# Kernel optimization log

Hardware: AMD Instinct MI355X
Metric: run time of the kernel (lower is better)

## Reference

```python
import math
import jax, jax.numpy as jnp
import numpy as np

EMBED_DIM = 2048
NUM_HEADS = 16
NUM_KV_HEADS = 8
DEPTH = 12
HEAD_DIM = EMBED_DIM // NUM_HEADS // 2  # 64
N_REP = NUM_HEADS // NUM_KV_HEADS       # 2
SCALING = HEAD_DIM ** (-0.5)
LAMBDA_INIT = 0.8 - 0.6 * math.exp(-0.3 * DEPTH)
EPS = 1e-5


def _rope_cos_sin(seq_len, head_dim, offset=0):
    pos = jnp.arange(offset, offset + seq_len, dtype=jnp.float32)
    theta = jnp.arange(0, head_dim, 2, dtype=jnp.float32) / head_dim
    inv_freq = 1.0 / (10000.0 ** theta + 1e-8)
    sinusoid = pos[:, None] * inv_freq[None, :]  # [seq, head_dim//2]
    return jnp.cos(sinusoid), jnp.sin(sinusoid)


def _apply_rotary_interleaved(x, cos, sin):
    # x: [b, s, h, d]; cos/sin: [s, d//2]; interleaved pairs (even, odd)
    x1 = x[..., 0::2]
    x2 = x[..., 1::2]
    c = cos[None, :, None, :]
    s = sin[None, :, None, :]
    o1 = x1 * c - x2 * s
    o2 = x1 * s + x2 * c
    return jnp.stack([o1, o2], axis=-1).reshape(x.shape)


def setup_inputs() -> dict:
    key = jax.random.key(0)
    ks = jax.random.split(key, 12)
    d = EMBED_DIM
    inp = {
        "q": jax.random.normal(ks[0], (1, 2048, d), dtype=jnp.float32),
        "k": jax.random.normal(ks[1], (1, 2048, d), dtype=jnp.float32),
        "v": jax.random.normal(ks[2], (1, 2048, d), dtype=jnp.float32),
        "Wq": jax.random.normal(ks[3], (d, d), dtype=jnp.float32) * (d ** -0.5),
        "Wk": jax.random.normal(ks[4], (d, d // N_REP), dtype=jnp.float32) * (d ** -0.5),
        "Wv": jax.random.normal(ks[5], (d, d // N_REP), dtype=jnp.float32) * (d ** -0.5),
        "Wout": jax.random.normal(ks[6], (d, d), dtype=jnp.float32) * (d ** -0.5),
        "lq1": jax.random.normal(ks[7], (HEAD_DIM,), dtype=jnp.float32) * 0.1,
        "lk1": jax.random.normal(ks[8], (HEAD_DIM,), dtype=jnp.float32) * 0.1,
        "lq2": jax.random.normal(ks[9], (HEAD_DIM,), dtype=jnp.float32) * 0.1,
        "lk2": jax.random.normal(ks[10], (HEAD_DIM,), dtype=jnp.float32) * 0.1,
        "subln_w": jnp.ones((2 * HEAD_DIM,), dtype=jnp.float32),
    }
    return inp


def reference(q, k, v, Wq, Wk, Wv, Wout, lq1, lk1, lq2, lk2, subln_w):
    bsz, tgt_len, _ = q.shape
    src_len = k.shape[1]
    hd = HEAD_DIM

    qp = (q @ Wq).reshape(bsz, tgt_len, 2 * NUM_HEADS, hd)
    kp = (k @ Wk).reshape(bsz, src_len, 2 * NUM_KV_HEADS, hd)
    vp = (v @ Wv).reshape(bsz, src_len, NUM_KV_HEADS, 2 * hd)

    q_cos, q_sin = _rope_cos_sin(tgt_len, hd)
    k_cos, k_sin = _rope_cos_sin(src_len, hd)
    qp = _apply_rotary_interleaved(qp, q_cos, q_sin)
    kp = _apply_rotary_interleaved(kp, k_cos, k_sin)

    qp = jnp.transpose(qp, (0, 2, 1, 3)) * SCALING          # [b, 2H, t, hd]
    kp = jnp.repeat(jnp.transpose(kp, (0, 2, 1, 3)), N_REP, axis=1)  # [b, 2H, s, hd]
    vp = jnp.repeat(jnp.transpose(vp, (0, 2, 1, 3)), N_REP, axis=1)  # [b, H, s, 2hd]

    attn_weights = jnp.einsum('bhtd,bhsd->bhts', qp, kp)
    attn_weights = jax.nn.softmax(attn_weights.astype(jnp.float32), axis=-1).astype(qp.dtype)

    lambda_1 = jnp.exp(jnp.sum(lq1 * lk1))
    lambda_2 = jnp.exp(jnp.sum(lq2 * lk2))
    lambda_full = lambda_1 - lambda_2 + LAMBDA_INIT

    attn_weights = attn_weights.reshape(bsz, NUM_HEADS, 2, tgt_len, src_len)
    attn_weights = attn_weights[:, :, 0] - lambda_full * attn_weights[:, :, 1]

    attn = jnp.einsum('bhts,bhsd->bhtd', attn_weights, vp)  # [b, H, t, 2hd]

    # RMSNorm over last dim with affine weight
    rms = jax.lax.rsqrt(jnp.mean(jnp.square(attn), axis=-1, keepdims=True) + EPS)
    attn = attn * rms * subln_w
    attn = attn * (1.0 - LAMBDA_INIT)

    attn = jnp.transpose(attn, (0, 2, 1, 3)).reshape(bsz, tgt_len, NUM_HEADS * 2 * hd)
    return attn @ Wout
```

## Files before the change

kernel.cpp:

```cpp
#include <hip/hip_runtime.h>

typedef unsigned short u16;
typedef unsigned int u32;
typedef float f32x4 __attribute__((ext_vector_type(4)));
typedef float f32x2 __attribute__((ext_vector_type(2)));
typedef unsigned int u32x2 __attribute__((ext_vector_type(2)));
typedef __bf16 bf16x8 __attribute__((ext_vector_type(8)));
typedef __bf16 bf16x4 __attribute__((ext_vector_type(4)));

#define LAMBDA_INIT_F 0.7836057665316245f
#define ONE_MINUS_LI  0.2163942334683755f
#define THR_LOG2 11.0f
#define Q_SCALE 0.18033688011112042f

__device__ __forceinline__ u16 f2b(float f) {
  union { float f; u32 u; } x; x.f = f;
  u32 r = x.u + 0x7fffu + ((x.u >> 16) & 1u);
  return (u16)(r >> 16);
}

__device__ __forceinline__ f32x4 mfma16(bf16x8 a, bf16x8 b, f32x4 c) {
  return __builtin_amdgcn_mfma_f32_16x16x32_bf16(a, b, c, 0, 0, 0);
}

__device__ __forceinline__ float fexp2(float x) { return __builtin_amdgcn_exp2f(x); }

__device__ __forceinline__ void gll16(const void* gp, void* lp) {
  __builtin_amdgcn_global_load_lds((__attribute__((address_space(1))) void*)(gp),
                                   (__attribute__((address_space(3))) void*)(lp),
                                   16, 0, 0);
}

__device__ __forceinline__ void trans_body2(const float* __restrict__ in,
                                            u16* __restrict__ out, int R, int C,
                                            int bxb, int byb) {
  __shared__ float tile[32][33];
  int bx = bxb * 32;
  int by = byb * 32;
  int tx = threadIdx.x & 31, ty = threadIdx.x >> 5;
#pragma unroll
  for (int i = 0; i < 32; i += 8)
    tile[ty + i][tx] = in[(size_t)(by + ty + i) * C + bx + tx];
  __syncthreads();
#pragma unroll
  for (int i = 0; i < 32; i += 8)
    out[(size_t)(bx + ty + i) * R + by + tx] = f2b(tile[tx][ty + i]);
}

__global__ __launch_bounds__(256) void prep_kernel(
    const float* __restrict__ q, const float* __restrict__ k, const float* __restrict__ v,
    u16* __restrict__ qb, u16* __restrict__ kb, u16* __restrict__ vb,
    f32x2* __restrict__ tbl,
    const float* __restrict__ Wq, u16* __restrict__ WqT,
    const float* __restrict__ Wk, u16* __restrict__ WkT,
    const float* __restrict__ Wv, u16* __restrict__ WvT,
    const float* __restrict__ Wo, u16* __restrict__ WoT) {
  int bid = blockIdx.x;
  if (bid < 6144) {
    int seg = bid >> 11;
    int i = (bid & 2047) * 256 + threadIdx.x;
    const float* in = seg == 0 ? q : (seg == 1 ? k : v);
    u16* out = seg == 0 ? qb : (seg == 1 ? kb : vb);
    const f32x4* p = (const f32x4*)(in + (size_t)i * 8);
    f32x4 a = p[0], b = p[1];
    union { u16 u[8]; f32x4 v; } o;
#pragma unroll
    for (int j = 0; j < 4; ++j) { o.u[j] = f2b(a[j]); o.u[4 + j] = f2b(b[j]); }
    *(f32x4*)(out + (size_t)i * 8) = o.v;
    return;
  }
  if (bid < 6400) {
    int idx = (bid - 6144) * 256 + threadIdx.x;
    int t = idx >> 5, j = idx & 31;
    float theta = (float)j * (1.0f / 32.0f);
    float denom = expf(theta * 9.210340371976184f);
    float invf = 1.0f / (denom + 1e-8f);
    float ang = (float)t * invf;
    tbl[idx] = (f32x2){cosf(ang), sinf(ang)};
    return;
  }
  int w = bid - 6400;
  if (w < 4096)      trans_body2(Wq, WqT, 2048, 2048, w & 63, w >> 6);
  else if (w < 6144) { w -= 4096; trans_body2(Wk, WkT, 2048, 1024, w & 31, w >> 5); }
  else if (w < 8192) { w -= 6144; trans_body2(Wv, WvT, 2048, 1024, w & 31, w >> 5); }
  else               { w -= 8192; trans_body2(Wo, WoT, 2048, 2048, w & 63, w >> 6); }
}

template <int MODE>
__device__ __forceinline__ void gemm_body(u16* As, u16* Bs,
                                          const u16* __restrict__ A,
                                          const u16* __restrict__ Bt,
                                          void* __restrict__ Cout,
                                          const f32x2* __restrict__ tbl,
                                          float scale,
                                          int N, int K, int bx, int by) {
  const int tid = threadIdx.x;
  const int lane = tid & 63;
  const int wave = tid >> 6;
  const int m0 = by * 128;
  const int n0 = bx * 128;
  const int wm = (wave >> 1) * 64;
  const int wn = (wave & 1) * 64;
  const int g = lane >> 4, c = lane & 15;

  f32x4 acc[4][4];
#pragma unroll
  for (int i = 0; i < 4; ++i)
#pragma unroll
    for (int j = 0; j < 4; ++j) acc[i][j] = (f32x4){0.f, 0.f, 0.f, 0.f};

  for (int k0 = 0; k0 < K; k0 += 64) {
    __syncthreads();
#pragma unroll
    for (int it = 0; it < 4; ++it) {
      int gi = it * 256 + tid;
      int R = gi >> 3;
      int lg = (gi & 7) ^ (R & 7);
      gll16(A + (size_t)(m0 + R) * K + k0 + lg * 8, As + gi * 8);
      gll16(Bt + (size_t)(n0 + R) * K + k0 + lg * 8, Bs + gi * 8);
    }
    __syncthreads();
#pragma unroll
    for (int kk = 0; kk < 2; ++kk) {
      bf16x8 af[4], bf[4];
#pragma unroll
      for (int i = 0; i < 4; ++i) {
        int ph = ((kk * 4 + g) ^ (c & 7)) * 8;
        af[i] = *(const bf16x8*)&As[(wm + i * 16 + c) * 64 + ph];
        bf[i] = *(const bf16x8*)&Bs[(wn + i * 16 + c) * 64 + ph];
      }
#pragma unroll
      for (int i = 0; i < 4; ++i)
#pragma unroll
        for (int j = 0; j < 4; ++j) acc[i][j] = mfma16(af[i], bf[j], acc[i][j]);
    }
  }

  if constexpr (MODE == 0) {
    float* C = (float*)Cout;
#pragma unroll
    for (int i = 0; i < 4; ++i)
#pragma unroll
      for (int j = 0; j < 4; ++j) {
        int mrow = m0 + wm + i * 16 + g * 4;
        int ncol = n0 + wn + j * 16 + c;
#pragma unroll
        for (int r = 0; r < 4; ++r) C[(size_t)(mrow + r) * N + ncol] = acc[i][j][r];
      }
  } else if constexpr (MODE == 1) {
    u16* Oh = (u16*)Cout;
    const bool even = (c & 1) == 0;
#pragma unroll
    for (int i = 0; i < 4; ++i)
#pragma unroll
      for (int j = 0; j < 4; ++j) {
        int mrow = m0 + wm + i * 16 + g * 4;
        int ncol = n0 + wn + j * 16 + c;
        int hh = ncol >> 6;
        int d = ncol & 63;
        int jd = d >> 1;
        f32x4 own = acc[i][j];
        f32x4 part;
#pragma unroll
        for (int r = 0; r < 4; ++r) part[r] = __shfl_xor(own[r], 1);
        if (even) {
#pragma unroll
          for (int r = 0; r < 4; ++r) {
            f32x2 cs = tbl[(mrow + r) * 32 + jd];
            float o1 = (own[r] * cs[0] - part[r] * cs[1]) * scale;
            float o2 = (own[r] * cs[1] + part[r] * cs[0]) * scale;
            u32 pk = (u32)f2b(o1) | ((u32)f2b(o2) << 16);
            *(u32*)&Oh[((size_t)hh * 2048 + mrow + r) * 64 + d] = pk;
          }
        }
      }
  } else {
    u16* Vt = (u16*)Cout;
#pragma unroll
    for (int i = 0; i < 4; ++i)
#pragma unroll
      for (int j = 0; j < 4; ++j) {
        int ncol = n0 + wn + j * 16 + c;
        int tblk = (m0 + wm + i * 16) >> 5;
        int p0 = 8 * g + 4 * (i & 1);
        u32x2 pk;
        pk[0] = (u32)f2b(acc[i][j][0]) | ((u32)f2b(acc[i][j][1]) << 16);
        pk[1] = (u32)f2b(acc[i][j][2]) | ((u32)f2b(acc[i][j][3]) << 16);
        *(u32x2*)&Vt[(size_t)ncol * 2048 + tblk * 32 + p0] = pk;
      }
  }
}

__global__ __launch_bounds__(256, 2) void gemm_qkv_kernel(
    const u16* __restrict__ qb, const u16* __restrict__ WqT, u16* __restrict__ Qh,
    const u16* __restrict__ kb, const u16* __restrict__ WkT, u16* __restrict__ Kh,
    const u16* __restrict__ vb, const u16* __restrict__ WvT, u16* __restrict__ Vt,
    const f32x2* __restrict__ tbl) {
  __shared__ u16 As[128 * 64];
  __shared__ u16 Bs[128 * 64];
  int bid = ((blockIdx.x & 7) << 6) | (blockIdx.x >> 3);
  if (bid < 256) {
    gemm_body<1>(As, Bs, qb, WqT, Qh, tbl, Q_SCALE, 2048, 2048, bid & 15, bid >> 4);
  } else if (bid < 384) {
    int t = bid - 256;
    gemm_body<1>(As, Bs, kb, WkT, Kh, tbl, 1.0f, 1024, 2048, t & 7, t >> 3);
  } else {
    int t = bid - 384;
    gemm_body<2>(As, Bs, vb, WvT, Vt, tbl, 1.0f, 1024, 2048, t & 7, t >> 3);
  }
}

__global__ __launch_bounds__(256, 2) void gemm_one_kernel(const u16* __restrict__ A,
                                                          const u16* __restrict__ Bt,
                                                          float* __restrict__ C) {
  __shared__ u16 As[128 * 64];
  __shared__ u16 Bs[128 * 64];
  int bid = ((blockIdx.x & 7) << 5) | (blockIdx.x >> 3);
  gemm_body<0>(As, Bs, A, Bt, C, nullptr, 1.0f, 2048, 2048, bid & 15, bid >> 4);
}

__global__ __launch_bounds__(256, 2) void attn_kernel(const u16* __restrict__ Qb,
                                                      const u16* __restrict__ Kb,
                                                      const u16* __restrict__ Vt,
                                                      u16* __restrict__ AO,
                                                      const float* __restrict__ lq1,
                                                      const float* __restrict__ lk1,
                                                      const float* __restrict__ lq2,
                                                      const float* __restrict__ lk2,
                                                      const float* __restrict__ subln) {
  const int b = ((blockIdx.x & 7) << 6) | (blockIdx.x >> 3);
  const int h = b >> 5;
  const int tid = threadIdx.x;
  const int wave = tid >> 6;
  const int lane = tid & 63;
  const int t0 = ((b & 31) * 4 + wave) * 16;
  const int g = lane >> 4, c = lane & 15;
  const int c7 = c & 7;

  __shared__ u16 smem[24576];

  const u16* Kh = Kb + (size_t)h * 2048 * 64;
  const u16* Vh = Vt + (size_t)(h >> 1) * 128 * 2048;

  float myl1 = lq1[lane] * lk1[lane];
  float myl2 = lq2[lane] * lk2[lane];
#pragma unroll
  for (int off = 32; off; off >>= 1) {
    myl1 += __shfl_xor(myl1, off);
    myl2 += __shfl_xor(myl2, off);
  }
  const float lambda_full = expf(myl1) - expf(myl2) + LAMBDA_INIT_F;

  bf16x8 qf[2][2];
#pragma unroll
  for (int e = 0; e < 2; ++e)
#pragma unroll
    for (int d = 0; d < 2; ++d)
      qf[e][d] = *(const bf16x8*)(Qb + ((size_t)(2 * h + e) * 2048 + t0 + c) * 64 + d * 32 + g * 8);

  const int kb0 = c * 64 + ((g ^ c7) * 8);
  const int kb1 = kb0 ^ 32;

  const u16* ksrc0;
  const u16* ksrc1;
  const u16* vsrc0;
  const u16* vsrc1;
  const u16* vsrc2;
  const u16* vsrc3;
  { int gi = tid;       int R = gi >> 3; ksrc0 = Kh + R * 64 + ((gi & 7) ^ (R & 7)) * 8; }
  { int gi = 256 + tid; int R = gi >> 3; ksrc1 = Kh + R * 64 + ((gi & 7) ^ (R & 7)) * 8; }
  { int gi = tid;       int R = gi >> 3; vsrc0 = Vh + (size_t)R * 2048 + ((gi & 7) ^ (R & 7)) * 8; }
  { int gi = 256 + tid; int R = gi >> 3; vsrc1 = Vh + (size_t)R * 2048 + ((gi & 7) ^ (R & 7)) * 8; }
  { int gi = 512 + tid; int R = gi >> 3; vsrc2 = Vh + (size_t)R * 2048 + ((gi & 7) ^ (R & 7)) * 8; }
  { int gi = 768 + tid; int R = gi >> 3; vsrc3 = Vh + (size_t)R * 2048 + ((gi & 7) ^ (R & 7)) * 8; }

  f32x4 O[2][8];
#pragma unroll
  for (int e = 0; e < 2; ++e)
#pragma unroll
    for (int f = 0; f < 8; ++f) O[e][f] = (f32x4){0.f, 0.f, 0.f, 0.f};
  float m0 = -1e30f, m1 = -1e30f, ls0 = 0.f, ls1 = 0.f;

#define STAGE(kOff, vOff, s0)                                         \
  do {                                                                \
    gll16(ksrc0 + (size_t)(s0) * 64, smem + (kOff) + tid * 8);        \
    gll16(ksrc1 + (size_t)(s0) * 64, smem + (kOff) + 2048 + tid * 8); \
    gll16(vsrc0 + (s0), smem + (vOff) + tid * 8);                     \
    gll16(vsrc1 + (s0), smem + (vOff) + 2048 + tid * 8);              \
    gll16(vsrc2 + (s0), smem + (vOff) + 4096 + tid * 8);              \
    gll16(vsrc3 + (s0), smem + (vOff) + 6144 + tid * 8);              \
  } while (0)

#define TILE(kOff, vOff)                                                      \
  do {                                                                        \
    bf16x8 kf[4][2];                                                          \
    _Pragma("unroll") for (int sf = 0; sf < 4; ++sf) {                        \
      kf[sf][0] = *(const bf16x8*)&smem[(kOff) + kb0 + sf * 1024];            \
      kf[sf][1] = *(const bf16x8*)&smem[(kOff) + kb1 + sf * 1024];            \
    }                                                                         \
    f32x4 sa[2][4];                                                           \
    _Pragma("unroll") for (int e = 0; e < 2; ++e)                             \
      _Pragma("unroll") for (int sf = 0; sf < 4; ++sf) {                      \
        f32x4 z = (f32x4){0.f, 0.f, 0.f, 0.f};                                \
        z = mfma16(kf[sf][0], qf[e][0], z);                                   \
        z = mfma16(kf[sf][1], qf[e][1], z);                                   \
        sa[e][sf] = z;                                                        \
      }                                                                       \
    bf16x8 vv0[8];                                                            \
    _Pragma("unroll") for (int f = 0; f < 8; ++f)                             \
      vv0[f] = *(const bf16x8*)&smem[(vOff) + kb0 + f * 1024];                \
    bf16x8 paf[2][2];                                                         \
    _Pragma("unroll") for (int e = 0; e < 2; ++e) {                           \
      float& m_e = e ? m1 : m0;                                               \
      float& ls_e = e ? ls1 : ls0;                                            \
      float mx = sa[e][0][0];                                                 \
      _Pragma("unroll") for (int sf = 0; sf < 4; ++sf)                        \
        _Pragma("unroll") for (int r = 0; r < 4; ++r)                         \
          mx = fmaxf(mx, sa[e][sf][r]);                                       \
      mx = fmaxf(mx, __shfl_xor(mx, 16));                                     \
      mx = fmaxf(mx, __shfl_xor(mx, 32));                                     \
      if (__any(mx > m_e + THR_LOG2)) {                                       \
        float mn = fmaxf(m_e, mx);                                            \
        float sc = fexp2(m_e - mn);                                           \
        m_e = mn;                                                             \
        ls_e *= sc;                                                           \
        float scr[4];                                                         \
        _Pragma("unroll") for (int r = 0; r < 4; ++r) scr[r] = __shfl(sc, g * 4 + r); \
        _Pragma("unroll") for (int ff = 0; ff < 8; ++ff)                      \
          _Pragma("unroll") for (int r = 0; r < 4; ++r) O[e][ff][r] *= scr[r]; \
      }                                                                       \
      float p[4][4];                                                          \
      float sum = 0.f;                                                        \
      _Pragma("unroll") for (int sf = 0; sf < 4; ++sf)                        \
        _Pragma("unroll") for (int r = 0; r < 4; ++r) {                       \
          float pv = fexp2(sa[e][sf][r] - m_e);                               \
          p[sf][r] = pv;                                                      \
          sum += pv;                                                          \
        }                                                                     \
      sum += __shfl_xor(sum, 16);                                             \
      sum += __shfl_xor(sum, 32);                                             \
      ls_e += sum;                                                            \
      paf[e][0] = (bf16x8){(__bf16)p[0][0], (__bf16)p[0][1], (__bf16)p[0][2], (__bf16)p[0][3], \
                           (__bf16)p[1][0], (__bf16)p[1][1], (__bf16)p[1][2], (__bf16)p[1][3]}; \
      paf[e][1] = (bf16x8){(__bf16)p[2][0], (__bf16)p[2][1], (__bf16)p[2][2], (__bf16)p[2][3], \
                           (__bf16)p[3][0], (__bf16)p[3][1], (__bf16)p[3][2], (__bf16)p[3][3]}; \
    }                                                                         \
    __builtin_amdgcn_s_setprio(1);                                            \
    bf16x8 vv1[8];                                                            \
    _Pragma("unroll") for (int f = 0; f < 8; ++f)                             \
      vv1[f] = *(const bf16x8*)&smem[(vOff) + kb1 + f * 1024];                \
    _Pragma("unroll") for (int f = 0; f < 8; ++f) {                           \
      O[0][f] = mfma16(paf[0][0], vv0[f], O[0][f]);                           \
      O[1][f] = mfma16(paf[1][0], vv0[f], O[1][f]);                           \
    }                                                                         \
    _Pragma("unroll") for (int f = 0; f < 8; ++f) {                           \
      O[0][f] = mfma16(paf[0][1], vv1[f], O[0][f]);                           \
      O[1][f] = mfma16(paf[1][1], vv1[f], O[1][f]);                           \
    }                                                                         \
    __builtin_amdgcn_s_setprio(0);                                            \
  } while (0)

  STAGE(0, 8192, 0);

#pragma unroll 1
  for (int t = 0; t < 32; t += 2) {
    __syncthreads();
    STAGE(4096, 16384, (t + 1) * 64);
    TILE(0, 8192);
    __syncthreads();
    if (t < 30) STAGE(0, 8192, (t + 2) * 64);
    TILE(4096, 16384);
  }

  float inv0 = 1.f / ls0, inv1 = 1.f / ls1;
  float i0[4], i1[4];
#pragma unroll
  for (int r = 0; r < 4; ++r) {
    i0[r] = __shfl(inv0, g * 4 + r);
    i1[r] = __shfl(inv1, g * 4 + r);
  }
  float res[8][4];
  float ss[4] = {0.f, 0.f, 0.f, 0.f};
#pragma unroll
  for (int f = 0; f < 8; ++f)
#pragma unroll
    for (int r = 0; r < 4; ++r) {
      float vv = O[0][f][r] * i0[r] - lambda_full * (O[1][f][r] * i1[r]);
      res[f][r] = vv;
      ss[r] += vv * vv;
    }
#pragma unroll
  for (int off = 1; off < 16; off <<= 1)
#pragma unroll
    for (int r = 0; r < 4; ++r) ss[r] += __shfl_xor(ss[r], off);
  float rms[4];
#pragma unroll
  for (int r = 0; r < 4; ++r)
    rms[r] = rsqrtf(ss[r] * (1.0f / 128.0f) + 1e-5f) * ONE_MINUS_LI;
  float w[8];
#pragma unroll
  for (int f = 0; f < 8; ++f) w[f] = subln[f * 16 + c];
#pragma unroll
  for (int f = 0; f < 8; ++f)
#pragma unroll
    for (int r = 0; r < 4; ++r)
      AO[(size_t)(t0 + g * 4 + r) * 2048 + h * 128 + f * 16 + c] = f2b(res[f][r] * rms[r] * w[f]);
}

extern "C" void kernel_launch(void* const* d_in, const int* in_sizes, int n_in,
                              void* d_out, int out_size, void* d_ws, size_t ws_size,
                              hipStream_t stream) {
  const float* q     = (const float*)d_in[0];
  const float* k     = (const float*)d_in[1];
  const float* v     = (const float*)d_in[2];
  const float* Wq    = (const float*)d_in[3];
  const float* Wk    = (const float*)d_in[4];
  const float* Wv    = (const float*)d_in[5];
  const float* Wout  = (const float*)d_in[6];
  const float* lq1   = (const float*)d_in[7];
  const float* lk1   = (const float*)d_in[8];
  const float* lq2   = (const float*)d_in[9];
  const float* lk2   = (const float*)d_in[10];
  const float* subln = (const float*)d_in[11];
  float* out = (float*)d_out;

  char* ws = (char*)d_ws;
  size_t off = 0;
  auto alloc = [&](size_t bytes) -> void* {
    void* p = ws + off;
    off += (bytes + 255) & ~(size_t)255;
    return p;
  };
  u16* qb  = (u16*)alloc(2048ull * 2048 * 2);
  u16* kb  = (u16*)alloc(2048ull * 2048 * 2);
  u16* vb  = (u16*)alloc(2048ull * 2048 * 2);
  u16* WqT = (u16*)alloc(2048ull * 2048 * 2);
  u16* WkT = (u16*)alloc(1024ull * 2048 * 2);
  u16* WvT = (u16*)alloc(1024ull * 2048 * 2);
  u16* WoT = (u16*)alloc(2048ull * 2048 * 2);
  f32x2* tbl = (f32x2*)alloc(2048ull * 32 * 8);
  u16* Qh  = (u16*)alloc(32ull * 2048 * 64 * 2);
  u16* Kh  = (u16*)alloc(16ull * 2048 * 64 * 2);
  u16* Vt  = (u16*)alloc(1024ull * 2048 * 2);
  u16* AO  = (u16*)alloc(2048ull * 2048 * 2);

  prep_kernel<<<18688, 256, 0, stream>>>(q, k, v, qb, kb, vb, tbl,
                                         Wq, WqT, Wk, WkT, Wv, WvT, Wout, WoT);
  gemm_qkv_kernel<<<512, 256, 0, stream>>>(qb, WqT, Qh, kb, WkT, Kh, vb, WvT, Vt, tbl);
  attn_kernel<<<512, 256, 0, stream>>>(Qh, Kh, Vt, AO, lq1, lk1, lq2, lk2, subln);
  gemm_one_kernel<<<256, 256, 0, stream>>>(AO, WoT, out);
}
```

Baseline: 159.0 us.

## Widen attention blocks to 8 waves and use 128x64 tiles for output GEMM

The attention kernel now runs 512-thread blocks (8 waves, 128 query rows per block) over 256 blocks, so each K/V tile staged in shared memory serves twice as many query rows and each thread issues fewer async loads per stage. The output projection GEMM switches to a new 128x64 tile body launched with 512 blocks, doubling the block count for better CU coverage on the 2048x2048 output. The trade-off is higher register pressure per block in attention with launch_bounds(512,2), plus more redundant A-tile loads in the narrower GEMM.

```diff
diff --git a/kernel.cpp b/kernel.cpp
--- a/kernel.cpp
+++ b/kernel.cpp
@@ -191,6 +191,68 @@
   }
 }
 
+__device__ __forceinline__ void gemm_body64(u16* As, u16* Bs,
+                                            const u16* __restrict__ A,
+                                            const u16* __restrict__ Bt,
+                                            float* __restrict__ C,
+                                            int N, int K, int bx, int by) {
+  const int tid = threadIdx.x;
+  const int lane = tid & 63;
+  const int wave = tid >> 6;
+  const int m0 = by * 128;
+  const int n0 = bx * 64;
+  const int wm = (wave >> 1) * 64;
+  const int wn = (wave & 1) * 32;
+  const int g = lane >> 4, c = lane & 15;
+
+  f32x4 acc[4][2];
+#pragma unroll
+  for (int i = 0; i < 4; ++i)
+#pragma unroll
+    for (int j = 0; j < 2; ++j) acc[i][j] = (f32x4){0.f, 0.f, 0.f, 0.f};
+
+  for (int k0 = 0; k0 < K; k0 += 64) {
+    __syncthreads();
+#pragma unroll
+    for (int it = 0; it < 4; ++it) {
+      int gi = it * 256 + tid;
+      int R = gi >> 3;
+      int lg = (gi & 7) ^ (R & 7);
+      gll16(A + (size_t)(m0 + R) * K + k0 + lg * 8, As + gi * 8);
+    }
+#pragma unroll
+    for (int it = 0; it < 2; ++it) {
+      int gi = it * 256 + tid;
+      int R = gi >> 3;
+      int lg = (gi & 7) ^ (R & 7);
+      gll16(Bt + (size_t)(n0 + R) * K + k0 + lg * 8, Bs + gi * 8);
+    }
+    __syncthreads();
+#pragma unroll
+    for (int kk = 0; kk < 2; ++kk) {
+      bf16x8 af[4], bf[2];
+      int ph = ((kk * 4 + g) ^ (c & 7)) * 8;
+#pragma unroll
+      for (int i = 0; i < 4; ++i) af[i] = *(const bf16x8*)&As[(wm + i * 16 + c) * 64 + ph];
+#pragma unroll
+      for (int j = 0; j < 2; ++j) bf[j] = *(const bf16x8*)&Bs[(wn + j * 16 + c) * 64 + ph];
+#pragma unroll
+      for (int i = 0; i < 4; ++i)
+#pragma unroll
+        for (int j = 0; j < 2; ++j) acc[i][j] = mfma16(af[i], bf[j], acc[i][j]);
+    }
+  }
+#pragma unroll
+  for (int i = 0; i < 4; ++i)
+#pragma unroll
+    for (int j = 0; j < 2; ++j) {
+      int mrow = m0 + wm + i * 16 + g * 4;
+      int ncol = n0 + wn + j * 16 + c;
+#pragma unroll
+      for (int r = 0; r < 4; ++r) C[(size_t)(mrow + r) * N + ncol] = acc[i][j][r];
+    }
+}
+
 __global__ __launch_bounds__(256, 2) void gemm_qkv_kernel(
     const u16* __restrict__ qb, const u16* __restrict__ WqT, u16* __restrict__ Qh,
     const u16* __restrict__ kb, const u16* __restrict__ WkT, u16* __restrict__ Kh,
@@ -214,12 +276,12 @@
                                                           const u16* __restrict__ Bt,
                                                           float* __restrict__ C) {
   __shared__ u16 As[128 * 64];
-  __shared__ u16 Bs[128 * 64];
-  int bid = ((blockIdx.x & 7) << 5) | (blockIdx.x >> 3);
-  gemm_body<0>(As, Bs, A, Bt, C, nullptr, 1.0f, 2048, 2048, bid & 15, bid >> 4);
-}
-
-__global__ __launch_bounds__(256, 2) void attn_kernel(const u16* __restrict__ Qb,
+  __shared__ u16 Bs[64 * 64];
+  int bid = ((blockIdx.x & 7) << 6) | (blockIdx.x >> 3);
+  gemm_body64(As, Bs, A, Bt, C, 2048, 2048, bid & 31, bid >> 5);
+}
+
+__global__ __launch_bounds__(512, 2) void attn_kernel(const u16* __restrict__ Qb,
                                                       const u16* __restrict__ Kb,
                                                       const u16* __restrict__ Vt,
                                                       u16* __restrict__ AO,
@@ -228,12 +290,12 @@
                                                       const float* __restrict__ lq2,
                                                       const float* __restrict__ lk2,
                                                       const float* __restrict__ subln) {
-  const int b = ((blockIdx.x & 7) << 6) | (blockIdx.x >> 3);
-  const int h = b >> 5;
+  const int b = ((blockIdx.x & 7) << 5) | (blockIdx.x >> 3);
+  const int h = b >> 4;
   const int tid = threadIdx.x;
   const int wave = tid >> 6;
   const int lane = tid & 63;
-  const int t0 = ((b & 31) * 4 + wave) * 16;
+  const int t0 = ((b & 15) * 8 + wave) * 16;
   const int g = lane >> 4, c = lane & 15;
   const int c7 = c & 7;
 
@@ -262,17 +324,11 @@
   const int kb1 = kb0 ^ 32;
 
   const u16* ksrc0;
-  const u16* ksrc1;
   const u16* vsrc0;
   const u16* vsrc1;
-  const u16* vsrc2;
-  const u16* vsrc3;
   { int gi = tid;       int R = gi >> 3; ksrc0 = Kh + R * 64 + ((gi & 7) ^ (R & 7)) * 8; }
-  { int gi = 256 + tid; int R = gi >> 3; ksrc1 = Kh + R * 64 + ((gi & 7) ^ (R & 7)) * 8; }
   { int gi = tid;       int R = gi >> 3; vsrc0 = Vh + (size_t)R * 2048 + ((gi & 7) ^ (R & 7)) * 8; }
-  { int gi = 256 + tid; int R = gi >> 3; vsrc1 = Vh + (size_t)R * 2048 + ((gi & 7) ^ (R & 7)) * 8; }
-  { int gi = 512 + tid; int R = gi >> 3; vsrc2 = Vh + (size_t)R * 2048 + ((gi & 7) ^ (R & 7)) * 8; }
-  { int gi = 768 + tid; int R = gi >> 3; vsrc3 = Vh + (size_t)R * 2048 + ((gi & 7) ^ (R & 7)) * 8; }
+  { int gi = 512 + tid; int R = gi >> 3; vsrc1 = Vh + (size_t)R * 2048 + ((gi & 7) ^ (R & 7)) * 8; }
 
   f32x4 O[2][8];
 #pragma unroll
@@ -281,14 +337,11 @@
     for (int f = 0; f < 8; ++f) O[e][f] = (f32x4){0.f, 0.f, 0.f, 0.f};
   float m0 = -1e30f, m1 = -1e30f, ls0 = 0.f, ls1 = 0.f;
 
-#define STAGE(kOff, vOff, s0)                                         \
-  do {                                                                \
-    gll16(ksrc0 + (size_t)(s0) * 64, smem + (kOff) + tid * 8);        \
-    gll16(ksrc1 + (size_t)(s0) * 64, smem + (kOff) + 2048 + tid * 8); \
-    gll16(vsrc0 + (s0), smem + (vOff) + tid * 8);                     \
-    gll16(vsrc1 + (s0), smem + (vOff) + 2048 + tid * 8);              \
-    gll16(vsrc2 + (s0), smem + (vOff) + 4096 + tid * 8);              \
-    gll16(vsrc3 + (s0), smem + (vOff) + 6144 + tid * 8);              \
+#define STAGE(kOff, vOff, s0)                                   \
+  do {                                                          \
+    gll16(ksrc0 + (size_t)(s0) * 64, smem + (kOff) + tid * 8);  \
+    gll16(vsrc0 + (s0), smem + (vOff) + tid * 8);               \
+    gll16(vsrc1 + (s0), smem + (vOff) + 4096 + tid * 8);        \
   } while (0)
 
 #define TILE(kOff, vOff)                                                      \
@@ -447,6 +500,6 @@
   prep_kernel<<<18688, 256, 0, stream>>>(q, k, v, qb, kb, vb, tbl,
                                          Wq, WqT, Wk, WkT, Wv, WvT, Wout, WoT);
   gemm_qkv_kernel<<<512, 256, 0, stream>>>(qb, WqT, Qh, kb, WkT, Kh, vb, WvT, Vt, tbl);
-  attn_kernel<<<512, 256, 0, stream>>>(Qh, Kh, Vt, AO, lq1, lk1, lq2, lk2, subln);
-  gemm_one_kernel<<<256, 256, 0, stream>>>(AO, WoT, out);
-}
+  attn_kernel<<<256, 512, 0, stream>>>(Qh, Kh, Vt, AO, lq1, lk1, lq2, lk2, subln);
+  gemm_one_kernel<<<512, 256, 0, stream>>>(AO, WoT, out);
+}
```

Result: faster. 150.4 us (-5.4%).
